# Kernel tuning notes

Hardware: AMD Instinct MI355X
Metric: run time of the kernel (lower is better)

The kernel has to match this reference:

```python
import jax, jax.numpy as jnp
import numpy as np

D = 1024      # model_dimension
H = 16        # num_heads
HD = D // H   # head_dimension (shared K/V head dim)
B, S = 2, 2048


def setup_inputs() -> dict:
    key = jax.random.key(0)
    ks = jax.random.split(key, 11)
    s = 0.02
    return {
        "q": jax.random.normal(ks[0], (B, S, D), jnp.float32),
        "k": jax.random.normal(ks[1], (B, S, D), jnp.float32),
        "v": jax.random.normal(ks[2], (B, S, D), jnp.float32),
        "Wq": jax.random.normal(ks[3], (D, D), jnp.float32) * s,
        "bq": jnp.zeros((D,), jnp.float32),
        "Wk": jax.random.normal(ks[4], (D, HD), jnp.float32) * s,
        "bk": jnp.zeros((HD,), jnp.float32),
        "Wv": jax.random.normal(ks[5], (D, HD), jnp.float32) * s,
        "bv": jnp.zeros((HD,), jnp.float32),
        "Wo": jax.random.normal(ks[6], (D, D), jnp.float32) * s,
        "bo": jnp.zeros((D,), jnp.float32),
    }


def reference(q, k, v, Wq, bq, Wk, bk, Wv, bv, Wo, bo):
    Bsz, Sq, Dm = q.shape
    # Q projection + split into heads: (B, H, Sq, HD)
    qh = (q @ Wq + bq).reshape(Bsz, Sq, H, HD).transpose(0, 2, 1, 3)
    # Shared single K/V head: (B, Sk, HD)
    kh = k @ Wk + bk
    vh = v @ Wv + bv
    # Scores (B, H, Sq, Sk), scaled then clamped as in the original
    scores = jnp.einsum('bhqd,bkd->bhqk', qh, kh) / jnp.sqrt(jnp.float32(HD))
    scores = jnp.clip(scores, -1e6, 1e6)
    attn = jax.nn.softmax(scores, axis=-1)
    out = jnp.einsum('bhqk,bkd->bhqd', attn, vh)
    out = out.transpose(0, 2, 1, 3).reshape(Bsz, Sq, Dm)
    return out @ Wo + bo
```

## Files before the change

### kernel.cpp

```cpp
#include <hip/hip_runtime.h>
#include <cstdint>
#include <cstddef>

typedef unsigned short u16;
typedef uint32_t u32;
typedef __bf16 bf16x8 __attribute__((ext_vector_type(8)));
typedef float  f32x4  __attribute__((ext_vector_type(4)));
typedef u16    u16x4  __attribute__((ext_vector_type(4)));

#define DEV static __device__ __forceinline__
#define MFMA16(a, b, c) __builtin_amdgcn_mfma_f32_16x16x32_bf16(a, b, c, 0, 0, 0)

DEV u16 f2bf(float x) {
  unsigned u = __float_as_uint(x);
  u += 0x7fffu + ((u >> 16) & 1u);
  return (u16)(u >> 16);
}

DEV u32 cvt_pk_bf16(float lo, float hi) {
  u32 r;
  asm("v_cvt_pk_bf16_f32 %0, %1, %2" : "=v"(r) : "v"(lo), "v"(hi));
  return r;
}

DEV void gload_lds16(const void* g, void* l) {
  __builtin_amdgcn_global_load_lds(
      (__attribute__((address_space(1))) void*)(void*)g,
      (__attribute__((address_space(3))) void*)l, 16, 0, 0);
}

__global__ void k_convert3(const float* __restrict__ a, const float* __restrict__ b,
                           const float* __restrict__ c, u16* __restrict__ oa,
                           u16* __restrict__ ob, u16* __restrict__ oc, int n4) {
  int i = blockIdx.x * blockDim.x + threadIdx.x;
  if (i >= n4) return;
  const float* src = blockIdx.y == 0 ? a : blockIdx.y == 1 ? b : c;
  u16* dst = blockIdx.y == 0 ? oa : blockIdx.y == 1 ? ob : oc;
  f32x4 f = reinterpret_cast<const f32x4*>(src)[i];
  u16x4 o;
  o[0] = f2bf(f[0]); o[1] = f2bf(f[1]); o[2] = f2bf(f[2]); o[3] = f2bf(f[3]);
  reinterpret_cast<u16x4*>(dst)[i] = o;
}

__global__ void k_transpose2(const float* __restrict__ in0, u16* __restrict__ out0,
                             const float* __restrict__ in1, u16* __restrict__ out1,
                             int R, int C) {
  __shared__ float tile[32][33];
  const float* in = blockIdx.z ? in1 : in0;
  u16* out = blockIdx.z ? out1 : out0;
  int bx = blockIdx.x * 32, by = blockIdx.y * 32;
  int tx = threadIdx.x, ty = threadIdx.y;
#pragma unroll
  for (int j = 0; j < 4; ++j)
    tile[ty + j * 8][tx] = in[(size_t)(by + ty + j * 8) * C + bx + tx];
  __syncthreads();
#pragma unroll
  for (int j = 0; j < 4; ++j)
    out[(size_t)(bx + ty + j * 8) * R + by + tx] = f2bf(tile[tx][ty + j * 8]);
}

template <bool OUT_BF16>
__global__ __launch_bounds__(512) void k_gemm128(const u16* __restrict__ A, const u16* __restrict__ Bt,
                                                 const float* __restrict__ bias, void* __restrict__ Cout,
                                                 int M, int N, int K, float scale) {
  __shared__ u16 As[2][128 * 32];
  __shared__ u16 Bs[2][128 * 32];
  const int tid = threadIdx.x, lane = tid & 63, wid = tid >> 6;
  const int s = blockIdx.x;
  const int xr = s & 7, t = s >> 3;
  const int bx = t & 7;
  const int by = (t >> 3) * 8 + xr;
  const int brow = by * 128, bcol = bx * 128;
  const int wr = (wid >> 2) * 64, wc = (wid & 3) * 32;

  const int e0 = wid * 512 + lane * 8;
  const u16* a0 = A + (size_t)(brow + (e0 >> 5)) * K + (e0 & 31);
  const u16* b0 = Bt + (size_t)(bcol + (e0 >> 5)) * K + (e0 & 31);

  auto STAGE = [&](int buf, int k0) {
    gload_lds16(a0 + k0, &As[buf][wid * 512]);
    gload_lds16(b0 + k0, &Bs[buf][wid * 512]);
  };

  f32x4 acc[4][2] = {};
  const int NK = K / 32;
  STAGE(0, 0);
#pragma unroll 1
  for (int ks = 0; ks < NK; ++ks) {
    if (ks + 1 < NK) {
      STAGE((ks + 1) & 1, (ks + 1) * 32);
      asm volatile("s_waitcnt vmcnt(2)\n\ts_barrier" ::: "memory");
    } else {
      asm volatile("s_waitcnt vmcnt(0)\n\ts_barrier" ::: "memory");
    }
    __builtin_amdgcn_sched_barrier(0);

    const u16* Ab = &As[ks & 1][0];
    const u16* Bb = &Bs[ks & 1][0];
    const int lr = lane & 15, lk = (lane >> 4) * 8;
    bf16x8 af[4], bfr[2];
#pragma unroll
    for (int m = 0; m < 4; ++m) af[m] = *(const bf16x8*)&Ab[(wr + m * 16 + lr) * 32 + lk];
#pragma unroll
    for (int n = 0; n < 2; ++n) bfr[n] = *(const bf16x8*)&Bb[(wc + n * 16 + lr) * 32 + lk];
    __builtin_amdgcn_s_setprio(1);
#pragma unroll
    for (int m = 0; m < 4; ++m)
#pragma unroll
      for (int n = 0; n < 2; ++n) acc[m][n] = MFMA16(af[m], bfr[n], acc[m][n]);
    __builtin_amdgcn_s_setprio(0);
    asm volatile("s_barrier" ::: "memory");
  }

  const int lr = lane & 15, lg = lane >> 4;
#pragma unroll
  for (int m = 0; m < 4; ++m)
#pragma unroll
    for (int n = 0; n < 2; ++n) {
      const int col = bcol + wc + n * 16 + lr;
      const float bv = bias ? bias[col] : 0.f;
#pragma unroll
      for (int r = 0; r < 4; ++r) {
        const int row = brow + wr + m * 16 + lg * 4 + r;
        float val = (acc[m][n][r] + bv) * scale;
        if constexpr (OUT_BF16) ((u16*)Cout)[(size_t)row * N + col] = f2bf(val);
        else ((float*)Cout)[(size_t)row * N + col] = val;
      }
    }
}

__global__ __launch_bounds__(256) void k_gemm64(const u16* __restrict__ A0, const u16* __restrict__ A1,
                                                const u16* __restrict__ Bt0, const u16* __restrict__ Bt1,
                                                const float* __restrict__ bias0, const float* __restrict__ bias1,
                                                u16* __restrict__ C0, u16* __restrict__ C1, int K) {
  __shared__ u16 As[64 * 32];
  __shared__ u16 Bs[64 * 32];
  const int sel = blockIdx.y;
  const u16* A = sel ? A1 : A0;
  const u16* Bt = sel ? Bt1 : Bt0;
  const float* bias = sel ? bias1 : bias0;
  const int tid = threadIdx.x, lane = tid & 63, wid = tid >> 6;
  const int brow = blockIdx.x * 64;
  const int e0 = wid * 512 + lane * 8;
  const u16* a0 = A + (size_t)(brow + (e0 >> 5)) * K + (e0 & 31);
  const u16* b0 = Bt + (size_t)(e0 >> 5) * K + (e0 & 31);
  u16* lA = As + wid * 512;
  u16* lB = Bs + wid * 512;
  f32x4 acc[4] = {};

  for (int k0 = 0; k0 < K; k0 += 32) {
    gload_lds16(a0 + k0, lA);
    gload_lds16(b0 + k0, lB);
    __syncthreads();
    const int lr = lane & 15, lk = (lane >> 4) * 8;
    bf16x8 af = *(const bf16x8*)&As[(wid * 16 + lr) * 32 + lk];
#pragma unroll
    for (int n = 0; n < 4; ++n) {
      bf16x8 bfr = *(const bf16x8*)&Bs[(n * 16 + lr) * 32 + lk];
      acc[n] = MFMA16(af, bfr, acc[n]);
    }
    __syncthreads();
  }

  const int lr = lane & 15, lg = lane >> 4;
#pragma unroll
  for (int n = 0; n < 4; ++n) {
    const int col = n * 16 + lr;
    const float bv = bias[col];
#pragma unroll
    for (int r = 0; r < 4; ++r) {
      const int row = brow + wid * 16 + lg * 4 + r;
      const float val = acc[n][r] + bv;
      if (sel)
        C1[((size_t)(row >> 11) * 64 + col) * 2048 + (row & 2047)] = f2bf(val);
      else
        C0[(size_t)row * 64 + col] = f2bf(val);
    }
  }
}

__global__ __launch_bounds__(512) void k_attn(const u16* __restrict__ Qh, const u16* __restrict__ Kh,
                                              const u16* __restrict__ VhT, u16* __restrict__ Out) {
  constexpr int S = 2048, D = 1024, NT = 32;
  __shared__ u16 Ks[2][64 * 64];
  __shared__ u16 Vs[2][64 * 64];
  __shared__ u16 Ps[8][16 * 64];
  const int lane = threadIdx.x & 63, wid = threadIdx.x >> 6;
  const int lr = lane & 15, lg = lane >> 4;
  const int q0 = blockIdx.x * 128;
  const int h = blockIdx.y, b = blockIdx.z;

  bf16x8 qf[2];
#pragma unroll
  for (int kk = 0; kk < 2; ++kk)
    qf[kk] = *(const bf16x8*)&Qh[(size_t)(b * S + q0 + wid * 16 + lr) * D + h * 64 + kk * 32 + lg * 8];

  const int r8 = lane >> 3, ssl = (lane & 7) ^ r8;
  const u16* ksrc = Kh + (size_t)(b * S + wid * 8 + r8) * 64 + ssl * 8;
  const u16* vsrc = VhT + (size_t)(b * 64 + wid * 8 + r8) * S + ssl * 8;

  float lsum = 0.f;
  f32x4 o[4] = {};
  u16* Pw = &Ps[wid][0];
  const int pswz = (lr & 7) << 3;

  auto STAGE = [&](int buf, int t) {
    gload_lds16(ksrc + (size_t)(t * 64) * 64, &Ks[buf][(wid * 8) * 64]);
    gload_lds16(vsrc + t * 64, &Vs[buf][(wid * 8) * 64]);
  };

  STAGE(0, 0);
#pragma unroll 1
  for (int t = 0; t < NT; ++t) {
    if (t + 1 < NT) {
      STAGE((t + 1) & 1, t + 1);
      asm volatile("s_waitcnt vmcnt(2)\n\ts_barrier" ::: "memory");
    } else {
      asm volatile("s_waitcnt vmcnt(0)\n\ts_barrier" ::: "memory");
    }
    __builtin_amdgcn_sched_barrier(0);

    const u16* Kb = &Ks[t & 1][0];
    const u16* Vb = &Vs[t & 1][0];

    f32x4 z[4] = {};
    __builtin_amdgcn_s_setprio(1);
#pragma unroll
    for (int kk = 0; kk < 2; ++kk)
#pragma unroll
      for (int ct = 0; ct < 4; ++ct) {
        const int row = ct * 16 + lr;
        bf16x8 kf = *(const bf16x8*)&Kb[row * 64 + (((kk * 4 + lg) ^ (row & 7)) << 3)];
        z[ct] = MFMA16(kf, qf[kk], z[ct]);
      }
    __builtin_amdgcn_s_setprio(0);

    float s = 0.f;
#pragma unroll
    for (int ct = 0; ct < 4; ++ct) {
      const float p0 = __builtin_amdgcn_exp2f(z[ct][0]);
      const float p1 = __builtin_amdgcn_exp2f(z[ct][1]);
      const float p2 = __builtin_amdgcn_exp2f(z[ct][2]);
      const float p3 = __builtin_amdgcn_exp2f(z[ct][3]);
      s += (p0 + p1) + (p2 + p3);
      uint2 pk;
      pk.x = cvt_pk_bf16(p0, p1);
      pk.y = cvt_pk_bf16(p2, p3);
      *(uint2*)&Pw[lr * 64 + ((ct * 16 + lg * 4) ^ pswz)] = pk;
    }
    lsum += s;

#pragma unroll
    for (int kk = 0; kk < 2; ++kk) {
      bf16x8 pa = *(const bf16x8*)&Pw[lr * 64 + ((kk * 32 + lg * 8) ^ pswz)];
      __builtin_amdgcn_s_setprio(1);
#pragma unroll
      for (int nt = 0; nt < 4; ++nt) {
        const int row = nt * 16 + lr;
        bf16x8 vf = *(const bf16x8*)&Vb[row * 64 + (((kk * 4 + lg) ^ (row & 7)) << 3)];
        o[nt] = MFMA16(pa, vf, o[nt]);
      }
      __builtin_amdgcn_s_setprio(0);
    }
    asm volatile("s_barrier" ::: "memory");
  }

  lsum += __shfl_xor(lsum, 16);
  lsum += __shfl_xor(lsum, 32);
  const float linv = 1.f / lsum;
#pragma unroll
  for (int r = 0; r < 4; ++r) {
    const float li = __shfl(linv, (lane & 48) | (lg * 4 + r));
    const size_t row = (size_t)(b * S + q0 + wid * 16 + lg * 4 + r);
#pragma unroll
    for (int nt = 0; nt < 4; ++nt)
      Out[row * D + h * 64 + nt * 16 + lr] = f2bf(o[nt][r] * li);
  }
}

extern "C" void kernel_launch(void* const* d_in, const int* in_sizes, int n_in,
                              void* d_out, int out_size, void* d_ws, size_t ws_size,
                              hipStream_t stream) {
  const float* q  = (const float*)d_in[0];
  const float* k  = (const float*)d_in[1];
  const float* v  = (const float*)d_in[2];
  const float* Wq = (const float*)d_in[3];
  const float* bq = (const float*)d_in[4];
  const float* Wk = (const float*)d_in[5];
  const float* bk = (const float*)d_in[6];
  const float* Wv = (const float*)d_in[7];
  const float* bv = (const float*)d_in[8];
  const float* Wo = (const float*)d_in[9];
  const float* bo = (const float*)d_in[10];
  float* out = (float*)d_out;

  constexpr int B = 2, S = 2048, D = 1024, H = 16, HDc = 64;
  constexpr int M = B * S;

  char* ws = (char*)d_ws;
  size_t off = 0;
  auto alloc = [&](size_t bytes) { char* p = ws + off; off += bytes; return p; };
  u16* q_bf = (u16*)alloc((size_t)M * D * 2);
  u16* k_bf = (u16*)alloc((size_t)M * D * 2);
  u16* v_bf = (u16*)alloc((size_t)M * D * 2);
  u16* WqT  = (u16*)alloc((size_t)D * D * 2);
  u16* WkvT = (u16*)alloc((size_t)2 * HDc * D * 2);
  u16* WoT  = (u16*)alloc((size_t)D * D * 2);
  u16* Qh   = (u16*)alloc((size_t)M * D * 2);
  u16* Kh   = (u16*)alloc((size_t)M * HDc * 2);
  u16* VhT  = (u16*)alloc((size_t)M * HDc * 2);
  u16* WkT = WkvT;
  u16* WvT = WkvT + (size_t)HDc * D;
  u16* AO = q_bf;

  {
    int n4 = M * D / 4;
    k_convert3<<<dim3((n4 + 255) / 256, 3), 256, 0, stream>>>(q, k, v, q_bf, k_bf, v_bf, n4);
  }
  k_transpose2<<<dim3(D / 32, D / 32, 2), dim3(32, 8), 0, stream>>>(Wq, WqT, Wo, WoT, D, D);
  k_transpose2<<<dim3(HDc / 32, D / 32, 2), dim3(32, 8), 0, stream>>>(Wk, WkT, Wv, WvT, D, HDc);
  k_gemm128<true><<<dim3((M / 128) * (D / 128)), 512, 0, stream>>>(q_bf, WqT, bq, Qh, M, D, D,
                                                                   0.125f * 1.44269504089f);
  k_gemm64<<<dim3(M / 64, 2), 256, 0, stream>>>(k_bf, v_bf, WkT, WvT, bk, bv, Kh, VhT, D);
  k_attn<<<dim3(S / 128, H, B), 512, 0, stream>>>(Qh, Kh, VhT, AO);
  k_gemm128<false><<<dim3((M / 128) * (D / 128)), 512, 0, stream>>>(AO, WoT, bo, out, M, D, D, 1.0f);
}
```

Before: 125.4 us.

## Fuse fp32-to-bf16 activation conversion into projection GEMM A-tile loads

Drops the separate k_convert3 pass over q, k and v. The Q projection GEMM and the K/V projection GEMM now read fp32 activations straight into registers, convert them to bf16 with v_cvt_pk_bf16, and write them into LDS, one K-step ahead of the MFMAs. k_gemm64 also gains double-buffered LDS, priority hints and a software pipeline. This removes a full extra read and write of three 16 MB fp32 tensors, but each GEMM now reads A at twice the width and handles A through registers instead of direct global-to-LDS loads.

```diff
diff --git a/kernel.cpp b/kernel.cpp
--- a/kernel.cpp
+++ b/kernel.cpp
@@ -7,6 +7,7 @@
 typedef __bf16 bf16x8 __attribute__((ext_vector_type(8)));
 typedef float  f32x4  __attribute__((ext_vector_type(4)));
 typedef u16    u16x4  __attribute__((ext_vector_type(4)));
+typedef u32    u32x4  __attribute__((ext_vector_type(4)));
 
 #define DEV static __device__ __forceinline__
 #define MFMA16(a, b, c) __builtin_amdgcn_mfma_f32_16x16x32_bf16(a, b, c, 0, 0, 0)
@@ -27,19 +28,6 @@
   __builtin_amdgcn_global_load_lds(
       (__attribute__((address_space(1))) void*)(void*)g,
       (__attribute__((address_space(3))) void*)l, 16, 0, 0);
-}
-
-__global__ void k_convert3(const float* __restrict__ a, const float* __restrict__ b,
-                           const float* __restrict__ c, u16* __restrict__ oa,
-                           u16* __restrict__ ob, u16* __restrict__ oc, int n4) {
-  int i = blockIdx.x * blockDim.x + threadIdx.x;
-  if (i >= n4) return;
-  const float* src = blockIdx.y == 0 ? a : blockIdx.y == 1 ? b : c;
-  u16* dst = blockIdx.y == 0 ? oa : blockIdx.y == 1 ? ob : oc;
-  f32x4 f = reinterpret_cast<const f32x4*>(src)[i];
-  u16x4 o;
-  o[0] = f2bf(f[0]); o[1] = f2bf(f[1]); o[2] = f2bf(f[2]); o[3] = f2bf(f[3]);
-  reinterpret_cast<u16x4*>(dst)[i] = o;
 }
 
 __global__ void k_transpose2(const float* __restrict__ in0, u16* __restrict__ out0,
@@ -59,8 +47,8 @@
     out[(size_t)(bx + ty + j * 8) * R + by + tx] = f2bf(tile[tx][ty + j * 8]);
 }
 
-template <bool OUT_BF16>
-__global__ __launch_bounds__(512) void k_gemm128(const u16* __restrict__ A, const u16* __restrict__ Bt,
+template <bool OUT_BF16, bool A_FP32>
+__global__ __launch_bounds__(512) void k_gemm128(const void* __restrict__ Ap, const u16* __restrict__ Bt,
                                                  const float* __restrict__ bias, void* __restrict__ Cout,
                                                  int M, int N, int K, float scale) {
   __shared__ u16 As[2][128 * 32];
@@ -74,22 +62,47 @@
   const int wr = (wid >> 2) * 64, wc = (wid & 3) * 32;
 
   const int e0 = wid * 512 + lane * 8;
-  const u16* a0 = A + (size_t)(brow + (e0 >> 5)) * K + (e0 & 31);
   const u16* b0 = Bt + (size_t)(bcol + (e0 >> 5)) * K + (e0 & 31);
-
-  auto STAGE = [&](int buf, int k0) {
-    gload_lds16(a0 + k0, &As[buf][wid * 512]);
-    gload_lds16(b0 + k0, &Bs[buf][wid * 512]);
+  const u16* a0bf = A_FP32 ? nullptr : (const u16*)Ap + (size_t)(brow + (e0 >> 5)) * K + (e0 & 31);
+  const float* a0f = A_FP32 ? (const float*)Ap + (size_t)(brow + (tid >> 2)) * K + (tid & 3) * 8 : nullptr;
+
+  f32x4 ra0, ra1;
+  auto LOADA = [&](int k0) {
+    ra0 = *(const f32x4*)(a0f + k0);
+    ra1 = *(const f32x4*)(a0f + k0 + 4);
+  };
+  auto WRITEA = [&](int buf) {
+    u32x4 w;
+    w[0] = cvt_pk_bf16(ra0[0], ra0[1]);
+    w[1] = cvt_pk_bf16(ra0[2], ra0[3]);
+    w[2] = cvt_pk_bf16(ra1[0], ra1[1]);
+    w[3] = cvt_pk_bf16(ra1[2], ra1[3]);
+    *(u32x4*)&As[buf][tid * 8] = w;
   };
 
   f32x4 acc[4][2] = {};
   const int NK = K / 32;
-  STAGE(0, 0);
+  if constexpr (A_FP32) {
+    LOADA(0);
+    gload_lds16(b0, &Bs[0][wid * 512]);
+    WRITEA(0);
+    LOADA(32);
+    asm volatile("s_waitcnt lgkmcnt(0)" ::: "memory");
+  } else {
+    gload_lds16(a0bf, &As[0][wid * 512]);
+    gload_lds16(b0, &Bs[0][wid * 512]);
+  }
 #pragma unroll 1
   for (int ks = 0; ks < NK; ++ks) {
     if (ks + 1 < NK) {
-      STAGE((ks + 1) & 1, (ks + 1) * 32);
-      asm volatile("s_waitcnt vmcnt(2)\n\ts_barrier" ::: "memory");
+      if constexpr (A_FP32) {
+        gload_lds16(b0 + (ks + 1) * 32, &Bs[(ks + 1) & 1][wid * 512]);
+        asm volatile("s_waitcnt vmcnt(3)\n\ts_barrier" ::: "memory");
+      } else {
+        gload_lds16(a0bf + (ks + 1) * 32, &As[(ks + 1) & 1][wid * 512]);
+        gload_lds16(b0 + (ks + 1) * 32, &Bs[(ks + 1) & 1][wid * 512]);
+        asm volatile("s_waitcnt vmcnt(2)\n\ts_barrier" ::: "memory");
+      }
     } else {
       asm volatile("s_waitcnt vmcnt(0)\n\ts_barrier" ::: "memory");
     }
@@ -109,7 +122,16 @@
 #pragma unroll
       for (int n = 0; n < 2; ++n) acc[m][n] = MFMA16(af[m], bfr[n], acc[m][n]);
     __builtin_amdgcn_s_setprio(0);
-    asm volatile("s_barrier" ::: "memory");
+
+    if constexpr (A_FP32) {
+      if (ks + 1 < NK) {
+        WRITEA((ks + 1) & 1);
+        if (ks + 2 < NK) LOADA((ks + 2) * 32);
+      }
+      asm volatile("s_waitcnt lgkmcnt(0)\n\ts_barrier" ::: "memory");
+    } else {
+      asm volatile("s_barrier" ::: "memory");
+    }
   }
 
   const int lr = lane & 15, lg = lane >> 4;
@@ -129,37 +151,70 @@
     }
 }
 
-__global__ __launch_bounds__(256) void k_gemm64(const u16* __restrict__ A0, const u16* __restrict__ A1,
+__global__ __launch_bounds__(256) void k_gemm64(const float* __restrict__ A0, const float* __restrict__ A1,
                                                 const u16* __restrict__ Bt0, const u16* __restrict__ Bt1,
                                                 const float* __restrict__ bias0, const float* __restrict__ bias1,
                                                 u16* __restrict__ C0, u16* __restrict__ C1, int K) {
-  __shared__ u16 As[64 * 32];
-  __shared__ u16 Bs[64 * 32];
+  __shared__ u16 As[2][64 * 32];
+  __shared__ u16 Bs[2][64 * 32];
   const int sel = blockIdx.y;
-  const u16* A = sel ? A1 : A0;
+  const float* Af = sel ? A1 : A0;
   const u16* Bt = sel ? Bt1 : Bt0;
   const float* bias = sel ? bias1 : bias0;
   const int tid = threadIdx.x, lane = tid & 63, wid = tid >> 6;
   const int brow = blockIdx.x * 64;
   const int e0 = wid * 512 + lane * 8;
-  const u16* a0 = A + (size_t)(brow + (e0 >> 5)) * K + (e0 & 31);
   const u16* b0 = Bt + (size_t)(e0 >> 5) * K + (e0 & 31);
-  u16* lA = As + wid * 512;
-  u16* lB = Bs + wid * 512;
+  const float* a0f = Af + (size_t)(brow + (tid >> 2)) * K + (tid & 3) * 8;
+
+  f32x4 ra0, ra1;
+  auto LOADA = [&](int k0) {
+    ra0 = *(const f32x4*)(a0f + k0);
+    ra1 = *(const f32x4*)(a0f + k0 + 4);
+  };
+  auto WRITEA = [&](int buf) {
+    u32x4 w;
+    w[0] = cvt_pk_bf16(ra0[0], ra0[1]);
+    w[1] = cvt_pk_bf16(ra0[2], ra0[3]);
+    w[2] = cvt_pk_bf16(ra1[0], ra1[1]);
+    w[3] = cvt_pk_bf16(ra1[2], ra1[3]);
+    *(u32x4*)&As[buf][tid * 8] = w;
+  };
+
   f32x4 acc[4] = {};
-
-  for (int k0 = 0; k0 < K; k0 += 32) {
-    gload_lds16(a0 + k0, lA);
-    gload_lds16(b0 + k0, lB);
-    __syncthreads();
+  const int NK = K / 32;
+  LOADA(0);
+  gload_lds16(b0, &Bs[0][wid * 512]);
+  WRITEA(0);
+  LOADA(32);
+  asm volatile("s_waitcnt lgkmcnt(0)" ::: "memory");
+#pragma unroll 1
+  for (int ks = 0; ks < NK; ++ks) {
+    if (ks + 1 < NK) {
+      gload_lds16(b0 + (ks + 1) * 32, &Bs[(ks + 1) & 1][wid * 512]);
+      asm volatile("s_waitcnt vmcnt(3)\n\ts_barrier" ::: "memory");
+    } else {
+      asm volatile("s_waitcnt vmcnt(0)\n\ts_barrier" ::: "memory");
+    }
+    __builtin_amdgcn_sched_barrier(0);
+
+    const u16* Ab = &As[ks & 1][0];
+    const u16* Bb = &Bs[ks & 1][0];
     const int lr = lane & 15, lk = (lane >> 4) * 8;
-    bf16x8 af = *(const bf16x8*)&As[(wid * 16 + lr) * 32 + lk];
+    bf16x8 af = *(const bf16x8*)&Ab[(wid * 16 + lr) * 32 + lk];
+    __builtin_amdgcn_s_setprio(1);
 #pragma unroll
     for (int n = 0; n < 4; ++n) {
-      bf16x8 bfr = *(const bf16x8*)&Bs[(n * 16 + lr) * 32 + lk];
+      bf16x8 bfr = *(const bf16x8*)&Bb[(n * 16 + lr) * 32 + lk];
       acc[n] = MFMA16(af, bfr, acc[n]);
     }
-    __syncthreads();
+    __builtin_amdgcn_s_setprio(0);
+
+    if (ks + 1 < NK) {
+      WRITEA((ks + 1) & 1);
+      if (ks + 2 < NK) LOADA((ks + 2) * 32);
+    }
+    asm volatile("s_waitcnt lgkmcnt(0)\n\ts_barrier" ::: "memory");
   }
 
   const int lr = lane & 15, lg = lane >> 4;
@@ -300,28 +355,21 @@
   char* ws = (char*)d_ws;
   size_t off = 0;
   auto alloc = [&](size_t bytes) { char* p = ws + off; off += bytes; return p; };
-  u16* q_bf = (u16*)alloc((size_t)M * D * 2);
-  u16* k_bf = (u16*)alloc((size_t)M * D * 2);
-  u16* v_bf = (u16*)alloc((size_t)M * D * 2);
   u16* WqT  = (u16*)alloc((size_t)D * D * 2);
   u16* WkvT = (u16*)alloc((size_t)2 * HDc * D * 2);
   u16* WoT  = (u16*)alloc((size_t)D * D * 2);
   u16* Qh   = (u16*)alloc((size_t)M * D * 2);
   u16* Kh   = (u16*)alloc((size_t)M * HDc * 2);
   u16* VhT  = (u16*)alloc((size_t)M * HDc * 2);
+  u16* AO   = (u16*)alloc((size_t)M * D * 2);
   u16* WkT = WkvT;
   u16* WvT = WkvT + (size_t)HDc * D;
-  u16* AO = q_bf;
-
-  {
-    int n4 = M * D / 4;
-    k_convert3<<<dim3((n4 + 255) / 256, 3), 256, 0, stream>>>(q, k, v, q_bf, k_bf, v_bf, n4);
-  }
+
   k_transpose2<<<dim3(D / 32, D / 32, 2), dim3(32, 8), 0, stream>>>(Wq, WqT, Wo, WoT, D, D);
   k_transpose2<<<dim3(HDc / 32, D / 32, 2), dim3(32, 8), 0, stream>>>(Wk, WkT, Wv, WvT, D, HDc);
-  k_gemm128<true><<<dim3((M / 128) * (D / 128)), 512, 0, stream>>>(q_bf, WqT, bq, Qh, M, D, D,
-                                                                   0.125f * 1.44269504089f);
-  k_gemm64<<<dim3(M / 64, 2), 256, 0, stream>>>(k_bf, v_bf, WkT, WvT, bk, bv, Kh, VhT, D);
+  k_gemm128<true, true><<<dim3((M / 128) * (D / 128)), 512, 0, stream>>>(q, WqT, bq, Qh, M, D, D,
+                                                                         0.125f * 1.44269504089f);
+  k_gemm64<<<dim3(M / 64, 2), 256, 0, stream>>>(k, v, WkT, WvT, bk, bv, Kh, VhT, D);
   k_attn<<<dim3(S / 128, H, B), 512, 0, stream>>>(Qh, Kh, VhT, AO);
-  k_gemm128<false><<<dim3((M / 128) * (D / 128)), 512, 0, stream>>>(AO, WoT, bo, out, M, D, D, 1.0f);
-}
+  k_gemm128<false, false><<<dim3((M / 128) * (D / 128)), 512, 0, stream>>>(AO, WoT, bo, out, M, D, D, 1.0f);
+}
```

After: 120.6 us. 1.04x faster.
